# Performance work log

Measured on AMD Instinct MI355X. Metric: run time of the kernel, lower is better.

The kernel has to match this reference:

```python
import jax, jax.numpy as jnp
import numpy as np
from jax import lax

DIM = 8          # per-head dim
HEADS = 32       # in_channels // dim * heads_ratio = 256 // 8
SCALE = 5        # multi-scale aggregation kernel
EPS = 1e-15


def _conv2d(x, w, groups=1, pad=0):
    # NCHW conv, stride 1, symmetric padding, no bias
    return lax.conv_general_dilated(
        x, w, window_strides=(1, 1), padding=[(pad, pad), (pad, pad)],
        dimension_numbers=('NCHW', 'OIHW', 'NCHW'), feature_group_count=groups)


def setup_inputs() -> dict:
    key = jax.random.key(0)
    ks = jax.random.split(key, 5)
    B, C, H, W = 8, 256, 64, 64
    td = HEADS * DIM                      # total_dim = 256
    x = jax.random.normal(ks[0], (B, C, H, W), jnp.float32)
    w_qkv = jax.random.normal(ks[1], (3 * td, C, 1, 1), jnp.float32) * 0.05
    w_dw = jax.random.normal(ks[2], (3 * td, 1, SCALE, SCALE), jnp.float32) * 0.05
    w_pw = jax.random.normal(ks[3], (3 * td, (3 * td) // (3 * HEADS), 1, 1), jnp.float32) * 0.1
    w_proj = jax.random.normal(ks[4], (C, td * 2, 1, 1), jnp.float32) * 0.05
    return {'x': x, 'w_qkv': w_qkv, 'w_dw': w_dw, 'w_pw': w_pw, 'w_proj': w_proj}


def reference(x, w_qkv, w_dw, w_pw, w_proj):
    B, C, H, W = x.shape
    td = HEADS * DIM
    # qkv projection (1x1 conv, no norm/activation)
    qkv = _conv2d(x, w_qkv)                                        # [B, 3*td, H, W]
    # multi-scale aggregation: depthwise 5x5 then grouped 1x1 (groups = 3*heads)
    agg = _conv2d(qkv, w_dw, groups=3 * td, pad=SCALE // 2)        # depthwise
    agg = _conv2d(agg, w_pw, groups=3 * HEADS)                     # grouped pointwise
    ms = jnp.concatenate([qkv, agg], axis=1)                       # [B, 2*3*td, H, W]
    # reshape to head-groups: [B, G, N, 3*dim] with G = 2*heads, N = H*W
    ms = ms.reshape(B, -1, 3 * DIM, H * W).transpose(0, 1, 3, 2)
    q, k, v = jnp.split(ms, 3, axis=-1)                            # each [B, G, N, d]
    q = jax.nn.relu(q)
    k = jax.nn.relu(k)
    v = jnp.pad(v, ((0, 0), (0, 0), (0, 0), (0, 1)), constant_values=1.0)  # [B,G,N,d+1]
    # linear attention in fp32 (inputs already fp32)
    kv = jnp.einsum('bgnd,bgne->bgde', k, v)                       # [B,G,d,d+1]
    out = jnp.einsum('bgnd,bgde->bgne', q, kv)                     # [B,G,N,d+1]
    out = out[..., :-1] / (out[..., -1:] + EPS)                    # [B,G,N,d]
    out = out.transpose(0, 1, 3, 2).reshape(B, -1, H, W)           # [B, 2*td, H, W]
    return _conv2d(out, w_proj)                                    # [B, C_out, H, W]
```

## Files before the change

### kernel.cpp

```cpp
#include <hip/hip_runtime.h>

#define N_PIX 4096
#define IMG_W 64
#define C_IN 256
#define TD3 768
#define N_B 8
#define N_G 64
#define C_OUT 256

typedef _Float16 f16;
typedef _Float16 half8 __attribute__((ext_vector_type(8)));
typedef _Float16 f16x4 __attribute__((ext_vector_type(4)));
typedef _Float16 f16x2 __attribute__((ext_vector_type(2)));
typedef float f32x4 __attribute__((ext_vector_type(4)));

__global__ __launch_bounds__(256) void k_prep(const float* __restrict__ x,
                                              const float* __restrict__ wq,
                                              const float* __restrict__ wp,
                                              f16* __restrict__ xh,
                                              f16* __restrict__ xl,
                                              f16* __restrict__ wqq_h,
                                              f16* __restrict__ wqq_l,
                                              f16* __restrict__ wqkv,
                                              f16* __restrict__ wph) {
  const int t = threadIdx.x;
  if (blockIdx.z == 8) {
    const int bid = blockIdx.x + 64 * blockIdx.y;
    for (int i = bid * 256 + t; i < TD3 * C_IN + C_OUT * 512; i += 65536) {
      if (i < TD3 * C_IN) {
        const int r = i >> 8, k = i & 255;
        const float v = wq[i];
        const f16 h = (f16)v;
        const int g = r / 24, j = r % 24;
        if (j < 8) {
          const int qi = g * 8 + j;
          wqq_h[qi * 256 + k] = h;
          wqq_l[qi * 256 + k] = (f16)(v - (float)h);
        } else {
          const int kvi = g * 16 + (j - 8);
          wqkv[kvi * 256 + k] = h;
        }
      } else {
        const int j = i - TD3 * C_IN;
        wph[j] = (f16)wp[j];
      }
    }
    return;
  }
  __shared__ float st[64][65];
  const int n0 = blockIdx.x * 64;
  const int k0 = blockIdx.y * 64;
  const size_t b = blockIdx.z;
  const float* xb = x + b * (size_t)C_IN * N_PIX;
#pragma unroll
  for (int i = 0; i < 16; ++i) {
    const int idx = t + i * 256;
    const int r = idx >> 6, c = idx & 63;
    st[r][c] = xb[(size_t)(k0 + r) * N_PIX + n0 + c];
  }
  __syncthreads();
#pragma unroll
  for (int i = 0; i < 8; ++i) {
    const int idx = t + i * 256;
    const int n = idx >> 5, k2 = (idx & 31) * 2;
    const float v0 = st[k2][n], v1 = st[k2 + 1][n];
    const f16 h0 = (f16)v0, h1 = (f16)v1;
    const size_t o = (b * N_PIX + n0 + n) * C_IN + k0 + k2;
    *(f16x2*)(xh + o) = (f16x2){h0, h1};
    *(f16x2*)(xl + o) = (f16x2){(f16)(v0 - (float)h0), (f16)(v1 - (float)h1)};
  }
}

__global__ __launch_bounds__(256) void k_gemmqkv(const f16* __restrict__ Ah,
                                                 const f16* __restrict__ Al,
                                                 const f16* __restrict__ Akv,
                                                 const f16* __restrict__ Bh,
                                                 const f16* __restrict__ Bl,
                                                 f16* __restrict__ C) {
  __shared__ f16 sm[2][16384];
  const int t = threadIdx.x;
  const int lane = t & 63;
  const int w = t >> 6;

  if (blockIdx.x < 512) {
    const int bid = blockIdx.x;
    const int swz = (bid & 7) * 64 + (bid >> 3);
    const int mt = swz % 2;
    const int rest = swz / 2;
    const int nt = rest & 31;
    const size_t bz = rest >> 5;
    const int m0 = mt * 128;
    const int n0 = nt * 128;
    const int K = C_IN;

    const f16* Bhb = Bh + bz * (size_t)N_PIX * K;
    const f16* Blb = Bl + bz * (size_t)N_PIX * K;
    f16* Cb = C + bz * (size_t)TD3 * N_PIX;

    f32x4 acc[4][4];
#pragma unroll
    for (int i = 0; i < 4; ++i)
#pragma unroll
      for (int j = 0; j < 4; ++j) acc[i][j] = (f32x4){0.f, 0.f, 0.f, 0.f};

    const int wm = w >> 1, wn = w & 1;
    const int fr = lane & 15;
    const int fk = (lane >> 4) * 8;

    const f16* gsrc[8];
    int sslot[8];
#pragma unroll
    for (int i = 0; i < 8; ++i) {
      const int s = w + i * 4;
      const int frag = s & 7;
      const f16* base;
      int row0;
      if (s < 8) {
        base = Ah; row0 = m0;
      } else if (s < 16) {
        base = Al; row0 = m0;
      } else if (s < 24) {
        base = Bhb; row0 = n0;
      } else {
        base = Blb; row0 = n0;
      }
      gsrc[i] = base + (size_t)(row0 + frag * 16 + fr) * K + fk;
      sslot[i] = s * 512;
    }

#pragma unroll
    for (int i = 0; i < 8; ++i)
      __builtin_amdgcn_global_load_lds(
          (const __attribute__((address_space(1))) unsigned int*)gsrc[i],
          (__attribute__((address_space(3))) unsigned int*)&sm[0][sslot[i]], 16, 0, 0);

    int cur = 0;
    for (int tt = 0; tt < 8; ++tt) {
      if (tt + 1 < 8) {
#pragma unroll
        for (int i = 0; i < 8; ++i)
          __builtin_amdgcn_global_load_lds(
              (const __attribute__((address_space(1))) unsigned int*)(gsrc[i] + (tt + 1) * 32),
              (__attribute__((address_space(3))) unsigned int*)&sm[cur ^ 1][sslot[i]], 16, 0, 0);
        asm volatile("s_waitcnt vmcnt(8)" ::: "memory");
      } else {
        asm volatile("s_waitcnt vmcnt(0)" ::: "memory");
      }
      __builtin_amdgcn_s_barrier();
      const f16* smb = sm[cur];
      half8 ah[4], al[4], bh[4], bl[4];
#pragma unroll
      for (int mi = 0; mi < 4; ++mi) {
        ah[mi] = *(const half8*)&smb[(wm * 4 + mi) * 512 + lane * 8];
        al[mi] = *(const half8*)&smb[(8 + wm * 4 + mi) * 512 + lane * 8];
      }
#pragma unroll
      for (int ni = 0; ni < 4; ++ni) {
        bh[ni] = *(const half8*)&smb[(16 + wn * 4 + ni) * 512 + lane * 8];
        bl[ni] = *(const half8*)&smb[(24 + wn * 4 + ni) * 512 + lane * 8];
      }
#pragma unroll
      for (int mi = 0; mi < 4; ++mi)
#pragma unroll
        for (int ni = 0; ni < 4; ++ni) {
          acc[mi][ni] = __builtin_amdgcn_mfma_f32_16x16x32_f16(ah[mi], bh[ni], acc[mi][ni], 0, 0, 0);
          acc[mi][ni] = __builtin_amdgcn_mfma_f32_16x16x32_f16(ah[mi], bl[ni], acc[mi][ni], 0, 0, 0);
          acc[mi][ni] = __builtin_amdgcn_mfma_f32_16x16x32_f16(al[mi], bh[ni], acc[mi][ni], 0, 0, 0);
        }
      __builtin_amdgcn_s_barrier();
      cur ^= 1;
    }
    const int cr = (lane >> 4) * 4;
    const int cc = lane & 15;
#pragma unroll
    for (int mi = 0; mi < 4; ++mi)
#pragma unroll
      for (int ni = 0; ni < 4; ++ni) {
#pragma unroll
        for (int r = 0; r < 4; ++r) {
          const int row = m0 + wm * 64 + mi * 16 + cr + r;
          const int ch = (row >> 3) * 24 + (row & 7);
          Cb[(size_t)ch * N_PIX + n0 + wn * 64 + ni * 16 + cc] = (f16)acc[mi][ni][r];
        }
      }
  } else {
    const int bid = blockIdx.x - 512;
    const int swz = (bid & 7) * 128 + (bid >> 3);
    const int mt = swz % 4;
    const int rest = swz / 4;
    const int nt = rest & 31;
    const size_t bz = rest >> 5;
    const int m0 = mt * 128;
    const int n0 = nt * 128;
    const int K = C_IN;

    const f16* Bb = Bh + bz * (size_t)N_PIX * K;
    f16* Cb = C + bz * (size_t)TD3 * N_PIX;

    f32x4 acc[4][4];
#pragma unroll
    for (int i = 0; i < 4; ++i)
#pragma unroll
      for (int j = 0; j < 4; ++j) acc[i][j] = (f32x4){0.f, 0.f, 0.f, 0.f};

    const int wm = w >> 1, wn = w & 1;
    const int fr2 = lane >> 3;
    const int fko = (lane & 7) * 8;
    const f16* gsrc[4][2];
    int sslot[4][2];
#pragma unroll
    for (int i = 0; i < 4; ++i) {
      const int s = w + i * 4;
      const int frag = s & 7;
      const f16* base = (s < 8) ? Akv : Bb;
      const int row0 = (s < 8) ? m0 : n0;
#pragma unroll
      for (int j = 0; j < 2; ++j) {
        gsrc[i][j] = base + (size_t)(row0 + frag * 16 + j * 8 + fr2) * K + fko;
        sslot[i][j] = s * 1024 + j * 512;
      }
    }

#pragma unroll
    for (int i = 0; i < 4; ++i)
#pragma unroll
      for (int j = 0; j < 2; ++j)
        __builtin_amdgcn_global_load_lds(
            (const __attribute__((address_space(1))) unsigned int*)gsrc[i][j],
            (__attribute__((address_space(3))) unsigned int*)&sm[0][sslot[i][j]], 16, 0, 0);

    int cur = 0;
    for (int tt = 0; tt < 4; ++tt) {
      if (tt + 1 < 4) {
#pragma unroll
        for (int i = 0; i < 4; ++i)
#pragma unroll
          for (int j = 0; j < 2; ++j)
            __builtin_amdgcn_global_load_lds(
                (const __attribute__((address_space(1))) unsigned int*)(gsrc[i][j] + (tt + 1) * 64),
                (__attribute__((address_space(3))) unsigned int*)&sm[cur ^ 1][sslot[i][j]], 16, 0, 0);
        asm volatile("s_waitcnt vmcnt(8)" ::: "memory");
      } else {
        asm volatile("s_waitcnt vmcnt(0)" ::: "memory");
      }
      __builtin_amdgcn_s_barrier();
      const f16* smb = sm[cur];
      const int fb = (lane & 15) * 64 + (lane >> 4) * 8;
      half8 av[4][2], bv[4][2];
#pragma unroll
      for (int mi = 0; mi < 4; ++mi)
#pragma unroll
        for (int kk = 0; kk < 2; ++kk)
          av[mi][kk] = *(const half8*)&smb[(wm * 4 + mi) * 1024 + fb + kk * 32];
#pragma unroll
      for (int ni = 0; ni < 4; ++ni)
#pragma unroll
        for (int kk = 0; kk < 2; ++kk)
          bv[ni][kk] = *(const half8*)&smb[(8 + wn * 4 + ni) * 1024 + fb + kk * 32];
#pragma unroll
      for (int kk = 0; kk < 2; ++kk)
#pragma unroll
        for (int mi = 0; mi < 4; ++mi)
#pragma unroll
          for (int ni = 0; ni < 4; ++ni)
            acc[mi][ni] = __builtin_amdgcn_mfma_f32_16x16x32_f16(av[mi][kk], bv[ni][kk], acc[mi][ni], 0, 0, 0);
      __builtin_amdgcn_s_barrier();
      cur ^= 1;
    }
    const int cr = (lane >> 4) * 4;
    const int cc = lane & 15;
#pragma unroll
    for (int mi = 0; mi < 4; ++mi)
#pragma unroll
      for (int ni = 0; ni < 4; ++ni) {
#pragma unroll
        for (int r = 0; r < 4; ++r) {
          const int row = m0 + wm * 64 + mi * 16 + cr + r;
          const int ch = (row >> 4) * 24 + 8 + (row & 15);
          Cb[(size_t)ch * N_PIX + n0 + wn * 64 + ni * 16 + cc] = (f16)acc[mi][ni][r];
        }
      }
  }
}

__global__ __launch_bounds__(256) void k_gemm1(const f16* __restrict__ A,
                                               const f16* __restrict__ B,
                                               float* __restrict__ C,
                                               int M, int K) {
  __shared__ f16 sm[2][16 * 1024];
  const int t = threadIdx.x;
  const int lane = t & 63;
  const int w = t >> 6;

  const int per = gridDim.x >> 3;
  const int swz = (blockIdx.x & 7) * per + (blockIdx.x >> 3);
  const int mtiles = M >> 7;
  const int mt = swz % mtiles;
  const int rest = swz / mtiles;
  const int nt = rest & 31;
  const size_t bz = rest >> 5;
  const int m0 = mt * 128;
  const int n0 = nt * 128;

  const f16* Bb = B + bz * (size_t)N_PIX * K;
  float* Cb = C + bz * (size_t)M * N_PIX;

  f32x4 acc[4][4];
#pragma unroll
  for (int i = 0; i < 4; ++i)
#pragma unroll
    for (int j = 0; j < 4; ++j) acc[i][j] = (f32x4){0.f, 0.f, 0.f, 0.f};

  const int wm = w >> 1, wn = w & 1;
  const int fr2 = lane >> 3;
  const int fko = (lane & 7) * 8;
  const f16* gsrc[4][2];
  int sslot[4][2];
#pragma unroll
  for (int i = 0; i < 4; ++i) {
    const int s = w + i * 4;
    const int frag = s & 7;
    const f16* base = (s < 8) ? A : Bb;
    const int row0 = (s < 8) ? m0 : n0;
#pragma unroll
    for (int j = 0; j < 2; ++j) {
      gsrc[i][j] = base + (size_t)(row0 + frag * 16 + j * 8 + fr2) * K + fko;
      sslot[i][j] = s * 1024 + j * 512;
    }
  }

#pragma unroll
  for (int i = 0; i < 4; ++i)
#pragma unroll
    for (int j = 0; j < 2; ++j)
      __builtin_amdgcn_global_load_lds(
          (const __attribute__((address_space(1))) unsigned int*)gsrc[i][j],
          (__attribute__((address_space(3))) unsigned int*)&sm[0][sslot[i][j]], 16, 0, 0);

  const int ntk = K / 64;
  int cur = 0;
  for (int tt = 0; tt < ntk; ++tt) {
    if (tt + 1 < ntk) {
#pragma unroll
      for (int i = 0; i < 4; ++i)
#pragma unroll
        for (int j = 0; j < 2; ++j)
          __builtin_amdgcn_global_load_lds(
              (const __attribute__((address_space(1))) unsigned int*)(gsrc[i][j] + (tt + 1) * 64),
              (__attribute__((address_space(3))) unsigned int*)&sm[cur ^ 1][sslot[i][j]], 16, 0, 0);
      asm volatile("s_waitcnt vmcnt(8)" ::: "memory");
    } else {
      asm volatile("s_waitcnt vmcnt(0)" ::: "memory");
    }
    __builtin_amdgcn_s_barrier();
    const f16* smb = sm[cur];
    const int fb = (lane & 15) * 64 + (lane >> 4) * 8;
    half8 av[4][2], bv[4][2];
#pragma unroll
    for (int mi = 0; mi < 4; ++mi)
#pragma unroll
      for (int kk = 0; kk < 2; ++kk)
        av[mi][kk] = *(const half8*)&smb[(wm * 4 + mi) * 1024 + fb + kk * 32];
#pragma unroll
    for (int ni = 0; ni < 4; ++ni)
#pragma unroll
      for (int kk = 0; kk < 2; ++kk)
        bv[ni][kk] = *(const half8*)&smb[(8 + wn * 4 + ni) * 1024 + fb + kk * 32];
#pragma unroll
    for (int kk = 0; kk < 2; ++kk)
#pragma unroll
      for (int mi = 0; mi < 4; ++mi)
#pragma unroll
        for (int ni = 0; ni < 4; ++ni)
          acc[mi][ni] = __builtin_amdgcn_mfma_f32_16x16x32_f16(av[mi][kk], bv[ni][kk], acc[mi][ni], 0, 0, 0);
    __builtin_amdgcn_s_barrier();
    cur ^= 1;
  }
  const int cr = (lane >> 4) * 4;
  const int cc = lane & 15;
#pragma unroll
  for (int mi = 0; mi < 4; ++mi)
#pragma unroll
    for (int ni = 0; ni < 4; ++ni) {
      float* p = Cb + (size_t)(m0 + wm * 64 + mi * 16 + cr) * N_PIX + n0 + wn * 64 + ni * 16 + cc;
#pragma unroll
      for (int r = 0; r < 4; ++r) p[(size_t)r * N_PIX] = acc[mi][ni][r];
    }
}

__global__ __launch_bounds__(256) void k_dw(const f16* __restrict__ qkv,
                                            const float* __restrict__ wdw,
                                            f16* __restrict__ dw) {
  __shared__ float sin_[68][72];
  const int t = threadIdx.x;
  const int bc = blockIdx.x;
  const int ch = bc % TD3;
  const f16* src = qkv + (size_t)bc * N_PIX;

  for (int i = t; i < 68 * 72 / 4; i += 256) ((f32x4*)sin_)[i] = (f32x4){0.f, 0.f, 0.f, 0.f};
  float wreg[25];
#pragma unroll
  for (int i = 0; i < 25; ++i) wreg[i] = wdw[(size_t)ch * 25 + i];
  __syncthreads();
  for (int i = t; i < 512; i += 256) {
    const int r = i >> 3, c8 = (i & 7) * 8;
    const half8 p = *(const half8*)(src + r * 64 + c8);
    f32x4 lo = {(float)p[0], (float)p[1], (float)p[2], (float)p[3]};
    f32x4 hi = {(float)p[4], (float)p[5], (float)p[6], (float)p[7]};
    *(f32x4*)&sin_[r + 2][c8 + 4] = lo;
    *(f32x4*)&sin_[r + 2][c8 + 8] = hi;
  }
  __syncthreads();

  const int c = t & 63;
  const int rg = t >> 6;
  const int r0 = rg * 16;
  float win[5][5];
#pragma unroll
  for (int r = 0; r < 4; ++r)
#pragma unroll
    for (int j = 0; j < 5; ++j) win[r][j] = sin_[r0 + r][c + 2 + j];
#pragma unroll
  for (int orow = 0; orow < 16; ++orow) {
    const int slot = (orow + 4) % 5;
#pragma unroll
    for (int j = 0; j < 5; ++j) win[slot][j] = sin_[r0 + orow + 4][c + 2 + j];
    float s = 0.f;
#pragma unroll
    for (int dr = 0; dr < 5; ++dr) {
      const int rs = (orow + dr) % 5;
#pragma unroll
      for (int dc = 0; dc < 5; ++dc) s = fmaf(win[rs][dc], wreg[dr * 5 + dc], s);
    }
    dw[(size_t)bc * N_PIX + (r0 + orow) * 64 + c] = (f16)s;
  }
}

__global__ __launch_bounds__(256) void k_pw(const f16* __restrict__ dw,
                                            const float* __restrict__ wpw,
                                            f16* __restrict__ agg) {
  const int t = threadIdx.x;
  const int q = blockIdx.x;
  const int bg = blockIdx.y;
  const int g = bg % 96;
  float wp[64];
#pragma unroll
  for (int i = 0; i < 64; ++i) wp[i] = wpw[(size_t)g * 64 + i];
  const size_t base = ((size_t)(bg / 96) * TD3 + g * 8) * N_PIX + q * 1024;
  const int px0 = t * 4;
  float dv[8][4];
#pragma unroll
  for (int ic = 0; ic < 8; ++ic) {
    const f16x4 v = *(const f16x4*)(dw + base + (size_t)ic * N_PIX + px0);
#pragma unroll
    for (int j = 0; j < 4; ++j) dv[ic][j] = (float)v[j];
  }
#pragma unroll
  for (int oc = 0; oc < 8; ++oc) {
    f16x4 o;
#pragma unroll
    for (int j = 0; j < 4; ++j) {
      float s = 0.f;
#pragma unroll
      for (int ic = 0; ic < 8; ++ic) s = fmaf(dv[ic][j], wp[oc * 8 + ic], s);
      o[j] = (f16)s;
    }
    *(f16x4*)(agg + base + (size_t)oc * N_PIX + px0) = o;
  }
}

__global__ __launch_bounds__(256, 1) void k_kv(const f16* __restrict__ qkv,
                                               const f16* __restrict__ agg,
                                               float* __restrict__ kvbuf) {
  const int t = threadIdx.x;
  const int g = blockIdx.x;
  const int b = blockIdx.y;
  const f16* src = (g < 32) ? qkv : agg;
  const int base = (g & 31) * 24;
  const f16* kc = src + ((size_t)b * TD3 + base + 8) * N_PIX;
  const f16* vc = src + ((size_t)b * TD3 + base + 16) * N_PIX;

  float acc[72];
#pragma unroll
  for (int i = 0; i < 72; i++) acc[i] = 0.f;

  for (int i = 0; i < N_PIX / 256; i++) {
    const int n = t + i * 256;
    float kd[8], ve[8];
#pragma unroll
    for (int d = 0; d < 8; d++) kd[d] = fmaxf((float)kc[(size_t)d * N_PIX + n], 0.f);
#pragma unroll
    for (int e = 0; e < 8; e++) ve[e] = (float)vc[(size_t)e * N_PIX + n];
#pragma unroll
    for (int d = 0; d < 8; d++) {
#pragma unroll
      for (int e = 0; e < 8; e++) acc[d * 9 + e] = fmaf(kd[d], ve[e], acc[d * 9 + e]);
      acc[d * 9 + 8] += kd[d];
    }
  }

  const int lane = t & 63, wv = t >> 6;
#pragma unroll
  for (int i = 0; i < 72; i++) acc[i] += __shfl_xor(acc[i], 32, 64);
  const int hi = lane >> 5;
  float r[36];
#pragma unroll
  for (int i = 0; i < 36; i++) r[i] = hi ? acc[36 + i] : acc[i];
#pragma unroll
  for (int off = 16; off >= 1; off >>= 1) {
#pragma unroll
    for (int i = 0; i < 36; i++) r[i] += __shfl_xor(r[i], off, 64);
  }
  __shared__ float red[4][72];
  if (lane == 0 || lane == 32) {
#pragma unroll
    for (int i = 0; i < 36; i++) red[wv][hi * 36 + i] = r[i];
  }
  __syncthreads();
  if (t < 72) {
    const float s = red[0][t] + red[1][t] + red[2][t] + red[3][t];
    kvbuf[((size_t)b * N_G + g) * 72 + t] = s;
  }
}

__global__ __launch_bounds__(256) void k_att(const f16* __restrict__ qkvh,
                                             const f16* __restrict__ aggh,
                                             const float* __restrict__ kvbuf,
                                             f16* __restrict__ atth) {
  __shared__ float skv[N_G * 72];
  __shared__ f16 sa[512][34];
  const int t = threadIdx.x;
  const int n0 = blockIdx.x * 32;
  const size_t b = blockIdx.y;
  for (int i = t; i < N_G * 72; i += 256) skv[i] = kvbuf[b * (N_G * 72) + i];
  __syncthreads();
  const int px = t & 31, gq = t >> 5;
#pragma unroll
  for (int gi = 0; gi < 8; ++gi) {
    const int g = gq * 8 + gi;
    const f16* src = (g < 32) ? qkvh : aggh;
    const int base = (g & 31) * 24;
    const f16* qc = src + ((size_t)b * TD3 + base) * N_PIX + n0 + px;
    float num[8] = {0.f, 0.f, 0.f, 0.f, 0.f, 0.f, 0.f, 0.f};
    float den = 0.f;
#pragma unroll
    for (int d = 0; d < 8; ++d) {
      const float qd = fmaxf((float)qc[(size_t)d * N_PIX], 0.f);
      const float* kvg = &skv[g * 72 + d * 9];
#pragma unroll
      for (int e = 0; e < 8; ++e) num[e] = fmaf(qd, kvg[e], num[e]);
      den = fmaf(qd, kvg[8], den);
    }
    const float rd = 1.f / (den + 1e-15f);
#pragma unroll
    for (int e = 0; e < 8; ++e) sa[g * 8 + e][px] = (f16)(num[e] * rd);
  }
  __syncthreads();
  f16* dst = atth + (b * N_PIX + n0) * 512;
  for (int i = 0; i < 64; ++i) {
    const int idx = t + i * 256;
    dst[idx] = sa[idx & 511][idx >> 9];
  }
}

extern "C" void kernel_launch(void* const* d_in, const int* in_sizes, int n_in,
                              void* d_out, int out_size, void* d_ws, size_t ws_size,
                              hipStream_t stream) {
  const float* x = (const float*)d_in[0];
  const float* w_qkv = (const float*)d_in[1];
  const float* w_dw = (const float*)d_in[2];
  const float* w_pw = (const float*)d_in[3];
  const float* w_proj = (const float*)d_in[4];
  float* out = (float*)d_out;

  char* ws = (char*)d_ws;
  size_t off = 0;
  f16* qkvh = (f16*)(ws + off); off += (size_t)N_B * TD3 * N_PIX * 2;
  f16* aggh = (f16*)(ws + off); off += (size_t)N_B * TD3 * N_PIX * 2;
  float* kvbuf = (float*)(ws + off); off += (size_t)N_B * N_G * 72 * 4;
  f16* wqq_h = (f16*)(ws + off); off += (size_t)256 * C_IN * 2;
  f16* wqq_l = (f16*)(ws + off); off += (size_t)256 * C_IN * 2;
  f16* wqkv = (f16*)(ws + off); off += (size_t)512 * C_IN * 2;
  f16* wph = (f16*)(ws + off); off += (size_t)C_OUT * 512 * 2;
  f16* xTh = (f16*)(ws + off);
  f16* xTl = xTh + (size_t)N_B * N_PIX * C_IN;
  f16* dwbuf = (f16*)(ws + off);
  f16* atth = (f16*)(ws + off);

  k_prep<<<dim3(N_PIX / 64, C_IN / 64, N_B + 1), 256, 0, stream>>>(
      x, w_qkv, w_proj, xTh, xTl, wqq_h, wqq_l, wqkv, wph);
  k_gemmqkv<<<dim3(512 + 1024), 256, 0, stream>>>(
      wqq_h, wqq_l, wqkv, xTh, xTl, qkvh);
  k_dw<<<dim3(N_B * TD3), 256, 0, stream>>>(qkvh, w_dw, dwbuf);
  k_pw<<<dim3(4, N_B * 96), 256, 0, stream>>>(dwbuf, w_pw, aggh);
  k_kv<<<dim3(N_G, N_B), 256, 0, stream>>>(qkvh, aggh, kvbuf);
  k_att<<<dim3(N_PIX / 32, N_B), 256, 0, stream>>>(qkvh, aggh, kvbuf, atth);
  k_gemm1<<<dim3(2 * 32 * N_B), 256, 0, stream>>>(wph, atth, out, C_OUT, 512);
}
```

Before: 143.3 us.

## Fuse grouped pointwise conv into kv reduction and attention kernels

Removes the separate k_pw kernel and its agg buffer. The grouped 1x1 is now applied on the fly: for keys it is computed per pixel inside k_kv, for values it is folded algebraically into the reduced kv matrix, and for queries it is computed per pixel inside k_att. This drops a full write and read pass of the aggregated tensor plus one launch, at the cost of extra FMAs and uncached global weight reads in k_att. dwbuf now gets its own workspace slot so it no longer aliases the transpose and attention scratch.

```diff
diff --git a/kernel.cpp b/kernel.cpp
--- a/kernel.cpp
+++ b/kernel.cpp
@@ -436,49 +436,27 @@
   }
 }
 
-__global__ __launch_bounds__(256) void k_pw(const f16* __restrict__ dw,
-                                            const float* __restrict__ wpw,
-                                            f16* __restrict__ agg) {
-  const int t = threadIdx.x;
-  const int q = blockIdx.x;
-  const int bg = blockIdx.y;
-  const int g = bg % 96;
-  float wp[64];
-#pragma unroll
-  for (int i = 0; i < 64; ++i) wp[i] = wpw[(size_t)g * 64 + i];
-  const size_t base = ((size_t)(bg / 96) * TD3 + g * 8) * N_PIX + q * 1024;
-  const int px0 = t * 4;
-  float dv[8][4];
-#pragma unroll
-  for (int ic = 0; ic < 8; ++ic) {
-    const f16x4 v = *(const f16x4*)(dw + base + (size_t)ic * N_PIX + px0);
-#pragma unroll
-    for (int j = 0; j < 4; ++j) dv[ic][j] = (float)v[j];
-  }
-#pragma unroll
-  for (int oc = 0; oc < 8; ++oc) {
-    f16x4 o;
-#pragma unroll
-    for (int j = 0; j < 4; ++j) {
-      float s = 0.f;
-#pragma unroll
-      for (int ic = 0; ic < 8; ++ic) s = fmaf(dv[ic][j], wp[oc * 8 + ic], s);
-      o[j] = (f16)s;
-    }
-    *(f16x4*)(agg + base + (size_t)oc * N_PIX + px0) = o;
-  }
-}
-
 __global__ __launch_bounds__(256, 1) void k_kv(const f16* __restrict__ qkv,
-                                               const f16* __restrict__ agg,
+                                               const f16* __restrict__ dw,
+                                               const float* __restrict__ wpw,
                                                float* __restrict__ kvbuf) {
   const int t = threadIdx.x;
   const int g = blockIdx.x;
   const int b = blockIdx.y;
-  const f16* src = (g < 32) ? qkv : agg;
-  const int base = (g & 31) * 24;
-  const f16* kc = src + ((size_t)b * TD3 + base + 8) * N_PIX;
-  const f16* vc = src + ((size_t)b * TD3 + base + 16) * N_PIX;
+  const bool pwp = (g >= 32);
+  __shared__ float swpk[64], swpv[64];
+  const f16 *kc, *vc;
+  if (pwp) {
+    const int gg = g - 32;
+    if (t < 64) swpk[t] = wpw[(size_t)(gg * 3 + 1) * 64 + t];
+    else if (t < 128) swpv[t - 64] = wpw[(size_t)(gg * 3 + 2) * 64 + (t - 64)];
+    kc = dw + ((size_t)b * TD3 + gg * 24 + 8) * N_PIX;
+    vc = dw + ((size_t)b * TD3 + gg * 24 + 16) * N_PIX;
+    __syncthreads();
+  } else {
+    kc = qkv + ((size_t)b * TD3 + g * 24 + 8) * N_PIX;
+    vc = qkv + ((size_t)b * TD3 + g * 24 + 16) * N_PIX;
+  }
 
   float acc[72];
 #pragma unroll
@@ -487,10 +465,25 @@
   for (int i = 0; i < N_PIX / 256; i++) {
     const int n = t + i * 256;
     float kd[8], ve[8];
-#pragma unroll
-    for (int d = 0; d < 8; d++) kd[d] = fmaxf((float)kc[(size_t)d * N_PIX + n], 0.f);
-#pragma unroll
-    for (int e = 0; e < 8; e++) ve[e] = (float)vc[(size_t)e * N_PIX + n];
+    if (pwp) {
+      float dk[8];
+#pragma unroll
+      for (int d = 0; d < 8; d++) dk[d] = (float)kc[(size_t)d * N_PIX + n];
+#pragma unroll
+      for (int e = 0; e < 8; e++) ve[e] = (float)vc[(size_t)e * N_PIX + n];
+#pragma unroll
+      for (int d = 0; d < 8; d++) {
+        float s = 0.f;
+#pragma unroll
+        for (int ic = 0; ic < 8; ic++) s = fmaf(dk[ic], swpk[d * 8 + ic], s);
+        kd[d] = fmaxf(s, 0.f);
+      }
+    } else {
+#pragma unroll
+      for (int d = 0; d < 8; d++) kd[d] = fmaxf((float)kc[(size_t)d * N_PIX + n], 0.f);
+#pragma unroll
+      for (int e = 0; e < 8; e++) ve[e] = (float)vc[(size_t)e * N_PIX + n];
+    }
 #pragma unroll
     for (int d = 0; d < 8; d++) {
 #pragma unroll
@@ -512,19 +505,31 @@
     for (int i = 0; i < 36; i++) r[i] += __shfl_xor(r[i], off, 64);
   }
   __shared__ float red[4][72];
+  __shared__ float fin[72];
   if (lane == 0 || lane == 32) {
 #pragma unroll
     for (int i = 0; i < 36; i++) red[wv][hi * 36 + i] = r[i];
   }
+  __syncthreads();
+  if (t < 72) fin[t] = red[0][t] + red[1][t] + red[2][t] + red[3][t];
   __syncthreads();
   if (t < 72) {
-    const float s = red[0][t] + red[1][t] + red[2][t] + red[3][t];
-    kvbuf[((size_t)b * N_G + g) * 72 + t] = s;
+    const int d = t / 9, e = t % 9;
+    float o;
+    if (!pwp || e == 8) {
+      o = fin[t];
+    } else {
+      o = 0.f;
+#pragma unroll
+      for (int ic = 0; ic < 8; ic++) o = fmaf(fin[d * 9 + ic], swpv[e * 8 + ic], o);
+    }
+    kvbuf[((size_t)b * N_G + g) * 72 + t] = o;
   }
 }
 
 __global__ __launch_bounds__(256) void k_att(const f16* __restrict__ qkvh,
-                                             const f16* __restrict__ aggh,
+                                             const f16* __restrict__ dw,
+                                             const float* __restrict__ wpw,
                                              const float* __restrict__ kvbuf,
                                              f16* __restrict__ atth) {
   __shared__ float skv[N_G * 72];
@@ -538,18 +543,37 @@
 #pragma unroll
   for (int gi = 0; gi < 8; ++gi) {
     const int g = gq * 8 + gi;
-    const f16* src = (g < 32) ? qkvh : aggh;
-    const int base = (g & 31) * 24;
-    const f16* qc = src + ((size_t)b * TD3 + base) * N_PIX + n0 + px;
     float num[8] = {0.f, 0.f, 0.f, 0.f, 0.f, 0.f, 0.f, 0.f};
     float den = 0.f;
-#pragma unroll
-    for (int d = 0; d < 8; ++d) {
-      const float qd = fmaxf((float)qc[(size_t)d * N_PIX], 0.f);
-      const float* kvg = &skv[g * 72 + d * 9];
-#pragma unroll
-      for (int e = 0; e < 8; ++e) num[e] = fmaf(qd, kvg[e], num[e]);
-      den = fmaf(qd, kvg[8], den);
+    const float* kvg0 = &skv[g * 72];
+    if (g < 32) {
+      const f16* qc = qkvh + ((size_t)b * TD3 + g * 24) * N_PIX + n0 + px;
+#pragma unroll
+      for (int d = 0; d < 8; ++d) {
+        const float qd = fmaxf((float)qc[(size_t)d * N_PIX], 0.f);
+        const float* kvg = kvg0 + d * 9;
+#pragma unroll
+        for (int e = 0; e < 8; ++e) num[e] = fmaf(qd, kvg[e], num[e]);
+        den = fmaf(qd, kvg[8], den);
+      }
+    } else {
+      const int gg = g - 32;
+      const f16* dc = dw + ((size_t)b * TD3 + gg * 24) * N_PIX + n0 + px;
+      const float* wq = wpw + (size_t)(gg * 3) * 64;
+      float dq[8];
+#pragma unroll
+      for (int ic = 0; ic < 8; ++ic) dq[ic] = (float)dc[(size_t)ic * N_PIX];
+#pragma unroll
+      for (int d = 0; d < 8; ++d) {
+        float s = 0.f;
+#pragma unroll
+        for (int ic = 0; ic < 8; ++ic) s = fmaf(dq[ic], wq[d * 8 + ic], s);
+        const float qd = fmaxf(s, 0.f);
+        const float* kvg = kvg0 + d * 9;
+#pragma unroll
+        for (int e = 0; e < 8; ++e) num[e] = fmaf(qd, kvg[e], num[e]);
+        den = fmaf(qd, kvg[8], den);
+      }
     }
     const float rd = 1.f / (den + 1e-15f);
 #pragma unroll
@@ -576,7 +600,7 @@
   char* ws = (char*)d_ws;
   size_t off = 0;
   f16* qkvh = (f16*)(ws + off); off += (size_t)N_B * TD3 * N_PIX * 2;
-  f16* aggh = (f16*)(ws + off); off += (size_t)N_B * TD3 * N_PIX * 2;
+  f16* dwbuf = (f16*)(ws + off); off += (size_t)N_B * TD3 * N_PIX * 2;
   float* kvbuf = (float*)(ws + off); off += (size_t)N_B * N_G * 72 * 4;
   f16* wqq_h = (f16*)(ws + off); off += (size_t)256 * C_IN * 2;
   f16* wqq_l = (f16*)(ws + off); off += (size_t)256 * C_IN * 2;
@@ -584,7 +608,6 @@
   f16* wph = (f16*)(ws + off); off += (size_t)C_OUT * 512 * 2;
   f16* xTh = (f16*)(ws + off);
   f16* xTl = xTh + (size_t)N_B * N_PIX * C_IN;
-  f16* dwbuf = (f16*)(ws + off);
   f16* atth = (f16*)(ws + off);
 
   k_prep<<<dim3(N_PIX / 64, C_IN / 64, N_B + 1), 256, 0, stream>>>(
@@ -592,8 +615,7 @@
   k_gemmqkv<<<dim3(512 + 1024), 256, 0, stream>>>(
       wqq_h, wqq_l, wqkv, xTh, xTl, qkvh);
   k_dw<<<dim3(N_B * TD3), 256, 0, stream>>>(qkvh, w_dw, dwbuf);
-  k_pw<<<dim3(4, N_B * 96), 256, 0, stream>>>(dwbuf, w_pw, aggh);
-  k_kv<<<dim3(N_G, N_B), 256, 0, stream>>>(qkvh, aggh, kvbuf);
-  k_att<<<dim3(N_PIX / 32, N_B), 256, 0, stream>>>(qkvh, aggh, kvbuf, atth);
+  k_kv<<<dim3(N_G, N_B), 256, 0, stream>>>(qkvh, dwbuf, w_pw, kvbuf);
+  k_att<<<dim3(N_PIX / 32, N_B), 256, 0, stream>>>(qkvh, dwbuf, w_pw, kvbuf, atth);
   k_gemm1<<<dim3(2 * 32 * N_B), 256, 0, stream>>>(wph, atth, out, C_OUT, 512);
 }
```

New measurement: 144.7 us. Within noise of the previous version (+1.0%).
